# Performance work log

Measured on AMD Instinct MI355X. Metric: run time of the kernel, lower is better.

Reference implementation:

```python
import jax, jax.numpy as jnp
import numpy as np

BETA = 0.25


def setup_inputs() -> dict:
    key = jax.random.key(0)
    k1, k2 = jax.random.split(key)
    n_e, dim_e = 1024, 256
    z = jax.random.normal(k1, (32, dim_e, 32, 32), dtype=jnp.float32)
    # nn.Embedding init: uniform(-1/n_e, 1/n_e)
    embeddings = jax.random.uniform(k2, (n_e, dim_e), dtype=jnp.float32,
                                    minval=-1.0 / n_e, maxval=1.0 / n_e)
    return {"z": z, "embeddings": embeddings}


def reference(z, embeddings):
    B, C, H, W = z.shape
    # (B,C,H,W) -> (B*H*W, C)
    z_flat = jnp.transpose(z, (0, 2, 3, 1)).reshape(-1, C)
    # squared L2 distances to every codebook vector: (N, n_e)
    distances = (jnp.sum(z_flat ** 2, axis=1, keepdims=True)
                 + jnp.sum(embeddings ** 2, axis=1)
                 - 2.0 * z_flat @ embeddings.T)
    idx = jnp.argmin(distances, axis=1)  # (N,)
    # quantized vectors, back to (B,C,H,W)
    z_q = embeddings[idx].reshape(B, H, W, C).transpose(0, 3, 1, 2)
    sg = jax.lax.stop_gradient
    loss = (jnp.mean((sg(z_q) - z) ** 2)
            + BETA * jnp.mean((z_q - sg(z)) ** 2))
    # module returns the index map (B,H,W) and the scalar loss
    return idx.reshape(B, H, W), loss
```

## Files before the change

kernel.cpp:

```cpp
#include <hip/hip_runtime.h>


#define NE   1024
#define DIM  256
#define BHW  32768
#define CST  1024
#define BST  262144
#define NTH  256
#define MT   128
#define NT   128
#define KT   16
#define RT   8
#define CTY  8
#define ZSTR 160
#define NKT  (DIM / KT)
#define GAP_MFMA 1.5e-4f
#define GAP_F32  2.5e-4f

#define OFF_SUME   0
#define OFF_LOSS   4096
#define OFF_CNT    4112
#define OFF_DONE   4120
#define OFF_T1     8192
#define OFF_BESTD  139264
#define OFF_LIST   270336
#define OFF_EMBT   401408
#define OFF_PART1  1449984
#define OFF_PART2  3547136
#define OFF_ZA     5242880
#define OFF_EB     38797312
#define WS_FAST_NEED 40894464ull

typedef unsigned long long ull;
typedef __attribute__((ext_vector_type(8))) short bf16x8;
typedef __attribute__((ext_vector_type(4))) float f32x4;

__device__ __forceinline__ unsigned short bf16rne(float x) {
    unsigned u = __float_as_uint(x);
    return (unsigned short)((u + 0x7fffu + ((u >> 16) & 1u)) >> 16);
}

__device__ __forceinline__ void gll16(const void* g, void* l) {
    __builtin_amdgcn_global_load_lds(
        (const __attribute__((address_space(1))) unsigned int*)g,
        (__attribute__((address_space(3))) unsigned int*)l, 16, 0, 0);
}

__device__ __forceinline__ float keyhi(ull k) {
    return __uint_as_float((unsigned)(k >> 32));
}
__device__ __forceinline__ void kmerge(ull& m1, float& m2, ull x1, float x2) {
    if (x1 < m1) { m2 = fminf(x2, keyhi(m1)); m1 = x1; }
    else          m2 = fminf(m2, keyhi(x1));
}

__device__ __forceinline__ float np_pw128_sq_contig(const float* p) {
    float r[8];
#pragma unroll
    for (int k = 0; k < 8; ++k) r[k] = __fmul_rn(p[k], p[k]);
    for (int i = 8; i < 128; i += 8) {
#pragma unroll
        for (int k = 0; k < 8; ++k)
            r[k] = __fadd_rn(r[k], __fmul_rn(p[i + k], p[i + k]));
    }
    return __fadd_rn(__fadd_rn(__fadd_rn(r[0], r[1]), __fadd_rn(r[2], r[3])),
                     __fadd_rn(__fadd_rn(r[4], r[5]), __fadd_rn(r[6], r[7])));
}

__global__ __launch_bounds__(NTH) void vq_prep(const float* __restrict__ emb,
                                               const float* __restrict__ z,
                                               float* __restrict__ sume,
                                               float* __restrict__ embT,
                                               unsigned short* __restrict__ Eb,
                                               unsigned short* __restrict__ Za,
                                               float* __restrict__ t1,
                                               double* __restrict__ loss_acc,
                                               int* __restrict__ cnt,
                                               int* __restrict__ done,
                                               int doEb) {
    __shared__ float zt[256 * 66];
    const int tid = threadIdx.x;

    if (blockIdx.x < 128) {
        if (blockIdx.x == 0 && tid == 0) { *loss_acc = 0.0; *cnt = 0; *done = 0; }
        const int j0   = blockIdx.x * 8;
        const int jloc = tid >> 5;
        const int c0   = (tid & 31) * 8;
        const int j    = j0 + jloc;

        const float4* gp = (const float4*)(emb + (size_t)j * DIM + c0);
        float4 v0 = gp[0], v1 = gp[1];
        float v[8] = {v0.x, v0.y, v0.z, v0.w, v1.x, v1.y, v1.z, v1.w};

#pragma unroll
        for (int k = 0; k < 8; ++k) zt[jloc * 264 + c0 + k] = v[k];

        if (doEb) {
            bf16x8 p1, p2;
#pragma unroll
            for (int k = 0; k < 8; ++k) {
                unsigned short b1 = bf16rne(v[k]);
                float b1f = __uint_as_float((unsigned)b1 << 16);
                unsigned short b2 = bf16rne(__fsub_rn(v[k], b1f));
                p1[k] = (short)b1;
                p2[k] = (short)b2;
            }
            const int kta = c0 >> 5, pos = c0 & 31;
            *(bf16x8*)(Eb + (size_t)kta * 32768 + (size_t)j * 32 + pos)       = p1;
            *(bf16x8*)(Eb + (size_t)(kta + 8) * 32768 + (size_t)j * 32 + pos) = p2;
        }
        __syncthreads();
        {
            float col[8];
#pragma unroll
            for (int r = 0; r < 8; ++r) col[r] = zt[r * 264 + tid];
            float4 w0 = {col[0], col[1], col[2], col[3]};
            float4 w1 = {col[4], col[5], col[6], col[7]};
            *(float4*)(embT + (size_t)tid * NE + j0)     = w0;
            *(float4*)(embT + (size_t)tid * NE + j0 + 4) = w1;
        }
        if (tid < 8) {
            const float* p = &zt[tid * 264];
            sume[j0 + tid] = __fadd_rn(np_pw128_sq_contig(p),
                                       np_pw128_sq_contig(p + 128));
        }
        return;
    }

    const int zb = blockIdx.x - 128;
    const int b = zb >> 4, hw0 = (zb & 15) * 64;
    const int idx = tid & 63, cq = tid >> 6;
    for (int c = cq * 64; c < cq * 64 + 64; ++c)
        zt[c * 66 + idx] = z[(size_t)b * BST + (size_t)c * CST + hw0 + idx];
    __syncthreads();
    if (tid < 64) {
        float r[8], h[2];
#pragma unroll
        for (int half = 0; half < 2; ++half) {
            int c0 = half * 128;
#pragma unroll
            for (int k = 0; k < 8; ++k) {
                float v = zt[(c0 + k) * 66 + tid];
                r[k] = __fmul_rn(v, v);
            }
            for (int c = 8; c < 128; ++c) {
                float v = zt[(c0 + c) * 66 + tid];
                r[c & 7] = __fadd_rn(r[c & 7], __fmul_rn(v, v));
            }
            h[half] = __fadd_rn(
                __fadd_rn(__fadd_rn(r[0], r[1]), __fadd_rn(r[2], r[3])),
                __fadd_rn(__fadd_rn(r[4], r[5]), __fadd_rn(r[6], r[7])));
        }
        t1[b * 1024 + hw0 + tid] = __fadd_rn(h[0], h[1]);
    }
    const int l = tid & 63, seg = tid >> 6;
    const int rloc = seg * 16 + (l >> 2), piece = l & 3;
    const int n = b * 1024 + hw0 + rloc;
    for (int kt = 0; kt < 16; ++kt) {
        bf16x8 pack;
        int cbase = (kt & 7) * 32 + piece * 8;
#pragma unroll
        for (int jj = 0; jj < 8; ++jj) {
            float zf = zt[(cbase + jj) * 66 + rloc];
            unsigned short a1 = bf16rne(zf);
            unsigned short v = a1;
            if (kt >= 8) {
                float a1f = __uint_as_float((unsigned)a1 << 16);
                v = bf16rne(__fsub_rn(zf, a1f));
            }
            pack[jj] = (short)v;
        }
        *(bf16x8*)(Za + (size_t)kt * 1048576 + (size_t)n * 32 + piece * 8) = pack;
    }
}

__global__ __launch_bounds__(NTH) void vq_mfma(const unsigned short* __restrict__ Za,
                                               const unsigned short* __restrict__ Eb,
                                               const float* __restrict__ sume,
                                               const float* __restrict__ t1g,
                                               ull* __restrict__ part1,
                                               float* __restrict__ part2) {
    __shared__ __align__(16) unsigned short As[8192];
    __shared__ __align__(16) unsigned short Bs[8192];
    __shared__ ull   red1[128];
    __shared__ float red2[128];

    const int tid = threadIdx.x;
    const int w = tid >> 6, lane = tid & 63;
    const int wr = w & 1, wc = w >> 1;
    const int c15 = lane & 15, q = lane >> 4;
    const int blk = blockIdx.x;
    const int ct = (blk >> 3) & 7;
    const int rowtile = ((blk >> 6) << 3) | (blk & 7);
    const int row0 = rowtile * MT;

    const int perm = (lane >> 2) * 32 + (((lane & 3) ^ ((lane >> 3) & 3)) * 8);
    const int qs = (q ^ ((c15 >> 1) & 3)) * 8;

    f32x4 acc[4][4];
#pragma unroll
    for (int i = 0; i < 4; ++i)
#pragma unroll
        for (int jb = 0; jb < 4; ++jb) acc[i][jb] = (f32x4){0.f, 0.f, 0.f, 0.f};

    const int s0 = w * 2;
    for (int ktp = 0; ktp < 8; ++ktp) {
        __syncthreads();
        {
            const unsigned short* gAlo = Za + (size_t)ktp * 1048576 + (size_t)row0 * 32;
            const unsigned short* gAhi = gAlo + 8u * 1048576u;
            const unsigned short* gBlo = Eb + (size_t)ktp * 32768 + (size_t)ct * 4096;
            const unsigned short* gBhi = gBlo + 8u * 32768u;
#pragma unroll
            for (int ss = 0; ss < 2; ++ss) {
                const int s = s0 + ss;
                gll16(gAlo + s * 512 + perm, (void*)&As[s * 512]);
                gll16(gAhi + s * 512 + perm, (void*)&As[4096 + s * 512]);
                gll16(gBlo + s * 512 + perm, (void*)&Bs[s * 512]);
                gll16(gBhi + s * 512 + perm, (void*)&Bs[4096 + s * 512]);
            }
        }
        __syncthreads();

        bf16x8 bl[4], bh[4];
#pragma unroll
        for (int jb = 0; jb < 4; ++jb) {
            const int nn = (wc * 64 + jb * 16 + c15) * 32 + qs;
            bl[jb] = *(const bf16x8*)&Bs[nn];
            bh[jb] = *(const bf16x8*)&Bs[4096 + nn];
        }
#pragma unroll
        for (int i = 0; i < 4; ++i) {
            const int mm = (wr * 64 + i * 16 + c15) * 32 + qs;
            bf16x8 al = *(const bf16x8*)&As[mm];
            bf16x8 ah = *(const bf16x8*)&As[4096 + mm];
#pragma unroll
            for (int jb = 0; jb < 4; ++jb) {
                acc[i][jb] = __builtin_amdgcn_mfma_f32_16x16x32_bf16(
                    al, bl[jb], acc[i][jb], 0, 0, 0);
                acc[i][jb] = __builtin_amdgcn_mfma_f32_16x16x32_bf16(
                    al, bh[jb], acc[i][jb], 0, 0, 0);
                acc[i][jb] = __builtin_amdgcn_mfma_f32_16x16x32_bf16(
                    ah, bl[jb], acc[i][jb], 0, 0, 0);
            }
        }
    }

    float sme[4];
#pragma unroll
    for (int jb = 0; jb < 4; ++jb)
        sme[jb] = sume[ct * 128 + wc * 64 + jb * 16 + c15];

    ull   mm1[4][4];
    float mm2[4][4];
#pragma unroll
    for (int i = 0; i < 4; ++i) {
#pragma unroll
        for (int reg = 0; reg < 4; ++reg) {
            int row = row0 + wr * 64 + i * 16 + q * 4 + reg;
            float t1v = t1g[row];
            ull m1 = ~0ull;
            float m2 = 3.4e38f;
#pragma unroll
            for (int jb = 0; jb < 4; ++jb) {
                float d = __fsub_rn(__fadd_rn(t1v, sme[jb]),
                                    __fmul_rn(2.0f, acc[i][jb][reg]));
                ull key = ((ull)__float_as_uint(d) << 32) |
                          (unsigned)(ct * 128 + wc * 64 + jb * 16 + c15);
                kmerge(m1, m2, key, 3.4e38f);
            }
#pragma unroll
            for (int m = 1; m < 16; m <<= 1) {
                ull x1 = __shfl_xor(m1, m);
                float x2 = __shfl_xor(m2, m);
                kmerge(m1, m2, x1, x2);
            }
            mm1[i][reg] = m1;
            mm2[i][reg] = m2;
        }
    }
    if (wc == 0 && c15 == 0) {
#pragma unroll
        for (int i = 0; i < 4; ++i)
#pragma unroll
            for (int reg = 0; reg < 4; ++reg) {
                red1[wr * 64 + i * 16 + q * 4 + reg] = mm1[i][reg];
                red2[wr * 64 + i * 16 + q * 4 + reg] = mm2[i][reg];
            }
    }
    __syncthreads();
    if (wc == 1 && c15 == 0) {
#pragma unroll
        for (int i = 0; i < 4; ++i)
#pragma unroll
            for (int reg = 0; reg < 4; ++reg) {
                int loc = wr * 64 + i * 16 + q * 4 + reg;
                ull m1 = mm1[i][reg];
                float m2 = mm2[i][reg];
                kmerge(m1, m2, red1[loc], red2[loc]);
                part1[(size_t)ct * BHW + row0 + loc] = m1;
                part2[(size_t)ct * BHW + row0 + loc] = m2;
            }
    }
}

__global__ __launch_bounds__(NTH) void vq_main_f32(const float* __restrict__ z,
                                                   const float* __restrict__ emb,
                                                   const float* __restrict__ sume,
                                                   const float* __restrict__ t1g,
                                                   ull* __restrict__ part1,
                                                   float* __restrict__ part2) {
    __shared__ __align__(16) char smem[25344];
    float* zs = (float*)smem;
    float* es = zs + KT * ZSTR;
    ull* red1 = (ull*)smem;
    float* red2 = (float*)(smem + 16896);

    const int tid = threadIdx.x;
    const int rowtile = blockIdx.x & 255;
    const int split = blockIdx.x >> 8;
    const int row0 = rowtile * MT;
    const int b = row0 >> 10;
    const int hw0 = row0 & 1023;
    const int rg = tid & 15, cg = tid >> 4;
    const int sm = tid & 127, skh = tid >> 7;
    const int sn = tid >> 1, skq = tid & 1;

    const float* zstg = z + (size_t)b * BST + hw0 + sm;
    const int zi = (sm >> 3) * 10 + (sm & 7);
    const int ei = (sn >> 3) * 10 + (sn & 7);

    float t1v[RT];
#pragma unroll
    for (int i = 0; i < RT; ++i) t1v[i] = t1g[row0 + rg * RT + i];

    ull b1[RT];
    float b2[RT];
#pragma unroll
    for (int i = 0; i < RT; ++i) { b1[i] = ~0ull; b2[i] = 3.4e38f; }

    const int code0 = split * NT;
    float accf[RT][CTY];
#pragma unroll
    for (int i = 0; i < RT; ++i)
#pragma unroll
        for (int j = 0; j < CTY; ++j) accf[i][j] = 0.0f;

    float smv[CTY];
#pragma unroll
    for (int j = 0; j < CTY; ++j) smv[j] = sume[code0 + cg * CTY + j];

    const float* estg = emb + (size_t)(code0 + sn) * DIM + skq * 8;

    for (int kt = 0; kt < NKT; ++kt) {
        __syncthreads();
        {
            const float* zp = zstg + (size_t)(kt * KT + skh) * CST;
#pragma unroll
            for (int kk = 0; kk < 8; ++kk)
                zs[(kk * 2 + skh) * ZSTR + zi] = zp[(size_t)(kk * 2) * CST];
        }
        {
            const float4* ep = (const float4*)(estg + kt * KT);
            float4 e0 = ep[0], e1 = ep[1];
            float ev[8] = {e0.x, e0.y, e0.z, e0.w, e1.x, e1.y, e1.z, e1.w};
#pragma unroll
            for (int qq = 0; qq < 8; ++qq)
                es[(skq * 8 + qq) * ZSTR + ei] = ev[qq];
        }
        __syncthreads();

#pragma unroll 2
        for (int k = 0; k < KT; ++k) {
            const float* zf = &zs[k * ZSTR + rg * 10];
            const float* ef = &es[k * ZSTR + cg * 10];
            float zr[RT], er[CTY];
#pragma unroll
            for (int i = 0; i < RT; ++i) zr[i] = zf[i];
#pragma unroll
            for (int j = 0; j < CTY; ++j) er[j] = ef[j];
#pragma unroll
            for (int i = 0; i < RT; ++i)
#pragma unroll
                for (int j = 0; j < CTY; ++j)
                    accf[i][j] = fmaf(zr[i], er[j], accf[i][j]);
        }
    }

#pragma unroll
    for (int i = 0; i < RT; ++i)
#pragma unroll
        for (int j = 0; j < CTY; ++j) {
            float d = __fsub_rn(__fadd_rn(t1v[i], smv[j]),
                                __fmul_rn(2.0f, accf[i][j]));
            ull key = ((ull)__float_as_uint(d) << 32) |
                      (unsigned)(code0 + cg * CTY + j);
            kmerge(b1[i], b2[i], key, 3.4e38f);
        }

    __syncthreads();
#pragma unroll
    for (int i = 0; i < RT; ++i) {
        red1[cg * 132 + rg * RT + i] = b1[i];
        red2[cg * 132 + rg * RT + i] = b2[i];
    }
    __syncthreads();
    if (tid < MT) {
        ull m1 = red1[tid];
        float m2 = red2[tid];
#pragma unroll
        for (int c = 1; c < 16; ++c)
            kmerge(m1, m2, red1[c * 132 + tid], red2[c * 132 + tid]);
        part1[(size_t)split * BHW + row0 + tid] = m1;
        part2[(size_t)split * BHW + row0 + tid] = m2;
    }
}

__global__ __launch_bounds__(NTH) void vq_t1(const float* __restrict__ z,
                                             float* __restrict__ t1) {
    int n = blockIdx.x * NTH + threadIdx.x;
    int b = n >> 10, hw = n & 1023;
    const float* p = z + (size_t)b * BST + hw;
    float r[8], h[2];
#pragma unroll
    for (int half = 0; half < 2; ++half) {
        int c0 = half * 128;
#pragma unroll
        for (int k = 0; k < 8; ++k) {
            float v = p[(size_t)(c0 + k) * CST];
            r[k] = __fmul_rn(v, v);
        }
        for (int c = 8; c < 128; ++c) {
            float v = p[(size_t)(c0 + c) * CST];
            r[c & 7] = __fadd_rn(r[c & 7], __fmul_rn(v, v));
        }
        h[half] = __fadd_rn(
            __fadd_rn(__fadd_rn(r[0], r[1]), __fadd_rn(r[2], r[3])),
            __fadd_rn(__fadd_rn(r[4], r[5]), __fadd_rn(r[6], r[7])));
    }
    t1[n] = __fadd_rn(h[0], h[1]);
}

__global__ __launch_bounds__(NTH) void vq_combine(const ull* __restrict__ part1,
                                                  const float* __restrict__ part2,
                                                  float* __restrict__ out,
                                                  float* __restrict__ bestd,
                                                  int* __restrict__ list,
                                                  int* __restrict__ cnt,
                                                  double* __restrict__ loss_acc,
                                                  float gapthr) {
    __shared__ double sdd[NTH];
    const int n = blockIdx.x * NTH + threadIdx.x;
    ull m1 = part1[n];
    float m2 = part2[n];
    for (int s = 1; s < 8; ++s)
        kmerge(m1, m2, part1[(size_t)s * BHW + n], part2[(size_t)s * BHW + n]);
    int j = (int)(m1 & 0xffffffffu);
    float d1 = keyhi(m1);
    out[n] = (float)j;
    bestd[n] = d1;
    float gap = __fsub_rn(m2, d1);
    if (!(gap >= gapthr)) {
        int p = atomicAdd(cnt, 1);
        list[p] = n;
    }
    sdd[threadIdx.x] = (double)d1;
    __syncthreads();
    for (int s = NTH / 2; s > 0; s >>= 1) {
        if (threadIdx.x < s) sdd[threadIdx.x] += sdd[threadIdx.x + s];
        __syncthreads();
    }
    if (threadIdx.x == 0) atomicAdd(loss_acc, sdd[0]);
}

__global__ __launch_bounds__(NTH) void vq_recheck(const float* __restrict__ z,
                                                  const float* __restrict__ embT,
                                                  const float* __restrict__ sume,
                                                  const float* __restrict__ t1g,
                                                  const int* __restrict__ list,
                                                  const int* __restrict__ cnt,
                                                  float* __restrict__ out,
                                                  const float* __restrict__ bestd,
                                                  double* __restrict__ loss_acc,
                                                  int* __restrict__ done) {
    __shared__ float zs[4][DIM];
    __shared__ ull sk[NTH];
    __shared__ int rows[4];
    const int t = threadIdx.x;
    int count = *cnt;
    if (count > BHW) count = BHW;
    const float4* ev = (const float4*)embT;
    const int nbatch = (count + 3) >> 2;

    for (int bi = blockIdx.x; bi < nbatch; bi += gridDim.x) {
        const int base = bi * 4;
        __syncthreads();
        if (t < 4) {
            int li = base + t;
            rows[t] = list[li < count ? li : count - 1];
        }
        __syncthreads();
        {
            int r = t >> 6, ci = t & 63;
            int n = rows[r], bb = n >> 10, hw = n & 1023;
#pragma unroll
            for (int k = 0; k < 4; ++k) {
                int c = ci + k * 64;
                zs[r][c] = z[(size_t)bb * BST + (size_t)c * CST + hw];
            }
        }
        __syncthreads();

        double acc[4][4];
#pragma unroll
        for (int r = 0; r < 4; ++r)
#pragma unroll
            for (int jj = 0; jj < 4; ++jj) acc[r][jj] = 0.0;

        for (int c0 = 0; c0 < DIM; c0 += 4) {
            float4 e[4];
#pragma unroll
            for (int u = 0; u < 4; ++u) e[u] = ev[(c0 + u) * 256 + t];
#pragma unroll
            for (int u = 0; u < 4; ++u) {
                double ex = (double)e[u].x, ey = (double)e[u].y;
                double ez = (double)e[u].z, ew = (double)e[u].w;
#pragma unroll
                for (int r = 0; r < 4; ++r) {
                    double zv = (double)zs[r][c0 + u];
                    acc[r][0] = fma(zv, ex, acc[r][0]);
                    acc[r][1] = fma(zv, ey, acc[r][1]);
                    acc[r][2] = fma(zv, ez, acc[r][2]);
                    acc[r][3] = fma(zv, ew, acc[r][3]);
                }
            }
        }

        const float4 sm = ((const float4*)sume)[t];
        const float smv[4] = {sm.x, sm.y, sm.z, sm.w};
#pragma unroll
        for (int r = 0; r < 4; ++r) {
            const int n = rows[r];
            const float t1v = t1g[n];
            ull bk = ~0ull;
#pragma unroll
            for (int jj = 0; jj < 4; ++jj) {
                int j = t * 4 + jj;
                float d = __fsub_rn(__fadd_rn(t1v, smv[jj]),
                                    __fmul_rn(2.0f, (float)acc[r][jj]));
                ull key = ((ull)__float_as_uint(d) << 32) | (unsigned)j;
                if (key < bk) bk = key;
            }
            sk[t] = bk;
            __syncthreads();
            for (int s = NTH / 2; s > 0; s >>= 1) {
                if (t < s) { ull o = sk[t + s]; if (o < sk[t]) sk[t] = o; }
                __syncthreads();
            }
            if (t == 0 && base + r < count) {
                int j = (int)(sk[0] & 0xffffffffu);
                out[n] = (float)j;
                atomicAdd(loss_acc, (double)keyhi(sk[0]) - (double)bestd[n]);
            }
            __syncthreads();
        }
    }

    if (t == 0) {
        __threadfence();
        int o = atomicAdd(done, 1);
        if (o == (int)gridDim.x - 1) {
            __threadfence();
            double total = atomicAdd(loss_acc, 0.0);
            double m = total / 8388608.0;
            float mf = (float)m;
            out[BHW] = __fadd_rn(mf, __fmul_rn(0.25f, mf));
        }
    }
}

extern "C" void kernel_launch(void* const* d_in, const int* in_sizes, int n_in,
                              void* d_out, int out_size, void* d_ws, size_t ws_size,
                              hipStream_t stream) {
    const float* z = (const float*)d_in[0];
    const float* emb = (const float*)d_in[1];
    float* out = (float*)d_out;

    char* ws = (char*)d_ws;
    float* sume = (float*)(ws + OFF_SUME);
    double* loss_acc = (double*)(ws + OFF_LOSS);
    int* cnt = (int*)(ws + OFF_CNT);
    int* done = (int*)(ws + OFF_DONE);
    float* t1 = (float*)(ws + OFF_T1);
    float* bestd = (float*)(ws + OFF_BESTD);
    int* list = (int*)(ws + OFF_LIST);
    float* embT = (float*)(ws + OFF_EMBT);
    ull* part1 = (ull*)(ws + OFF_PART1);
    float* part2 = (float*)(ws + OFF_PART2);
    unsigned short* Za = (unsigned short*)(ws + OFF_ZA);
    unsigned short* Eb = (unsigned short*)(ws + OFF_EB);

    const bool fast = ws_size >= WS_FAST_NEED;

    if (fast) {
        vq_prep<<<640, NTH, 0, stream>>>(emb, z, sume, embT, Eb, Za, t1,
                                         loss_acc, cnt, done, 1);
        vq_mfma<<<2048, NTH, 0, stream>>>(Za, Eb, sume, t1, part1, part2);
    } else {
        vq_prep<<<128, NTH, 0, stream>>>(emb, z, sume, embT, Eb, Za, t1,
                                         loss_acc, cnt, done, 0);
        vq_t1<<<BHW / NTH, NTH, 0, stream>>>(z, t1);
        vq_main_f32<<<2048, NTH, 0, stream>>>(z, emb, sume, t1, part1, part2);
    }
    vq_combine<<<BHW / NTH, NTH, 0, stream>>>(part1, part2, out, bestd, list, cnt,
                                              loss_acc, fast ? GAP_MFMA : GAP_F32);
    vq_recheck<<<2048, NTH, 0, stream>>>(z, embT, sume, t1, list, cnt, out, bestd,
                                         loss_acc, done);
}
```

Measured before the change: 251.8 us.

## Recheck ambiguous rows with fp32 filter then exact fp64 on candidates only

The recheck kernel now computes distances for all 1024 codes in fp32 instead of fp64. It keeps only the codes within a margin of the previous best distance and recomputes those few candidates in fp64, reducing the winner with a shared atomicMin. It also software-prefetches the next embedding chunk in the fp32 loop. This cuts the expensive fp64 FMA work and the per-row tree reductions, but correctness now depends on the fp32 filter margin being wide enough to keep the true minimum.

```diff
diff --git a/kernel.cpp b/kernel.cpp
--- a/kernel.cpp
+++ b/kernel.cpp
@@ -16,6 +16,7 @@
 #define NKT  (DIM / KT)
 #define GAP_MFMA 1.5e-4f
 #define GAP_F32  2.5e-4f
+#define CAND_MARGIN 1.0e-4f
 
 #define OFF_SUME   0
 #define OFF_LOSS   4096
@@ -474,6 +475,7 @@
 }
 
 __global__ __launch_bounds__(NTH) void vq_recheck(const float* __restrict__ z,
+                                                  const float* __restrict__ emb,
                                                   const float* __restrict__ embT,
                                                   const float* __restrict__ sume,
                                                   const float* __restrict__ t1g,
@@ -484,8 +486,11 @@
                                                   double* __restrict__ loss_acc,
                                                   int* __restrict__ done) {
     __shared__ float zs[4][DIM];
-    __shared__ ull sk[NTH];
-    __shared__ int rows[4];
+    __shared__ int   rows[4];
+    __shared__ float bds[4];
+    __shared__ ull   skrow[4];
+    __shared__ int   cand[4096];
+    __shared__ int   lcnt;
     const int t = threadIdx.x;
     int count = *cnt;
     if (count > BHW) count = BHW;
@@ -497,8 +502,12 @@
         __syncthreads();
         if (t < 4) {
             int li = base + t;
-            rows[t] = list[li < count ? li : count - 1];
-        }
+            int n = list[li < count ? li : count - 1];
+            rows[t] = n;
+            bds[t] = bestd[n];
+            skrow[t] = ~0ull;
+        }
+        if (t == 0) lcnt = 0;
         __syncthreads();
         {
             int r = t >> 6, ci = t & 63;
@@ -511,58 +520,79 @@
         }
         __syncthreads();
 
-        double acc[4][4];
+        float af[4][4];
 #pragma unroll
         for (int r = 0; r < 4; ++r)
 #pragma unroll
-            for (int jj = 0; jj < 4; ++jj) acc[r][jj] = 0.0;
-
+            for (int jj = 0; jj < 4; ++jj) af[r][jj] = 0.0f;
+
+        float4 e[4];
+#pragma unroll
+        for (int u = 0; u < 4; ++u) e[u] = ev[u * 256 + t];
         for (int c0 = 0; c0 < DIM; c0 += 4) {
-            float4 e[4];
-#pragma unroll
-            for (int u = 0; u < 4; ++u) e[u] = ev[(c0 + u) * 256 + t];
+            float4 en[4];
+            const int cn = (c0 + 4) & (DIM - 1);
+#pragma unroll
+            for (int u = 0; u < 4; ++u) en[u] = ev[(cn + u) * 256 + t];
 #pragma unroll
             for (int u = 0; u < 4; ++u) {
-                double ex = (double)e[u].x, ey = (double)e[u].y;
-                double ez = (double)e[u].z, ew = (double)e[u].w;
+                float ex = e[u].x, ey = e[u].y, ez = e[u].z, ew = e[u].w;
 #pragma unroll
                 for (int r = 0; r < 4; ++r) {
-                    double zv = (double)zs[r][c0 + u];
-                    acc[r][0] = fma(zv, ex, acc[r][0]);
-                    acc[r][1] = fma(zv, ey, acc[r][1]);
-                    acc[r][2] = fma(zv, ez, acc[r][2]);
-                    acc[r][3] = fma(zv, ew, acc[r][3]);
+                    float zv = zs[r][c0 + u];
+                    af[r][0] = fmaf(zv, ex, af[r][0]);
+                    af[r][1] = fmaf(zv, ey, af[r][1]);
+                    af[r][2] = fmaf(zv, ez, af[r][2]);
+                    af[r][3] = fmaf(zv, ew, af[r][3]);
                 }
             }
+#pragma unroll
+            for (int u = 0; u < 4; ++u) e[u] = en[u];
         }
 
         const float4 sm = ((const float4*)sume)[t];
         const float smv[4] = {sm.x, sm.y, sm.z, sm.w};
 #pragma unroll
         for (int r = 0; r < 4; ++r) {
-            const int n = rows[r];
-            const float t1v = t1g[n];
-            ull bk = ~0ull;
+            const float t1v = t1g[rows[r]];
+            const float lim = bds[r] + CAND_MARGIN;
 #pragma unroll
             for (int jj = 0; jj < 4; ++jj) {
-                int j = t * 4 + jj;
-                float d = __fsub_rn(__fadd_rn(t1v, smv[jj]),
-                                    __fmul_rn(2.0f, (float)acc[r][jj]));
-                ull key = ((ull)__float_as_uint(d) << 32) | (unsigned)j;
-                if (key < bk) bk = key;
-            }
-            sk[t] = bk;
-            __syncthreads();
-            for (int s = NTH / 2; s > 0; s >>= 1) {
-                if (t < s) { ull o = sk[t + s]; if (o < sk[t]) sk[t] = o; }
-                __syncthreads();
-            }
-            if (t == 0 && base + r < count) {
-                int j = (int)(sk[0] & 0xffffffffu);
-                out[n] = (float)j;
-                atomicAdd(loss_acc, (double)keyhi(sk[0]) - (double)bestd[n]);
-            }
-            __syncthreads();
+                float d = (t1v + smv[jj]) - 2.0f * af[r][jj];
+                if (d <= lim) {
+                    int p = atomicAdd(&lcnt, 1);
+                    cand[p] = (r << 10) | (t * 4 + jj);
+                }
+            }
+        }
+        __syncthreads();
+        const int nc = lcnt;
+
+        for (int ci = t; ci < nc; ci += NTH) {
+            int pk = cand[ci];
+            int r = pk >> 10, j = pk & 1023;
+            const float4* ep = (const float4*)(emb + (size_t)j * DIM);
+            double acc = 0.0;
+            for (int c4 = 0; c4 < 64; ++c4) {
+                float4 e4 = ep[c4];
+                acc = fma((double)zs[r][c4 * 4 + 0], (double)e4.x, acc);
+                acc = fma((double)zs[r][c4 * 4 + 1], (double)e4.y, acc);
+                acc = fma((double)zs[r][c4 * 4 + 2], (double)e4.z, acc);
+                acc = fma((double)zs[r][c4 * 4 + 3], (double)e4.w, acc);
+            }
+            float t1v = t1g[rows[r]];
+            float d = __fsub_rn(__fadd_rn(t1v, sume[j]),
+                                __fmul_rn(2.0f, (float)acc));
+            ull key = ((ull)__float_as_uint(d) << 32) | (unsigned)j;
+            atomicMin(&skrow[r], key);
+        }
+        __syncthreads();
+        if (t < 4 && base + t < count) {
+            ull k = skrow[t];
+            int n = rows[t];
+            int j = (int)(k & 0xffffffffu);
+            out[n] = (float)j;
+            atomicAdd(loss_acc, (double)keyhi(k) - (double)bds[t]);
         }
     }
 
@@ -614,6 +644,6 @@
     }
     vq_combine<<<BHW / NTH, NTH, 0, stream>>>(part1, part2, out, bestd, list, cnt,
                                               loss_acc, fast ? GAP_MFMA : GAP_F32);
-    vq_recheck<<<2048, NTH, 0, stream>>>(z, embT, sume, t1, list, cnt, out, bestd,
-                                         loss_acc, done);
-}
+    vq_recheck<<<2048, NTH, 0, stream>>>(z, emb, embT, sume, t1, list, cnt, out,
+                                         bestd, loss_acc, done);
+}
```

After: 273.2 us. 8.5% more time.
